# Kernel optimization log

Hardware: AMD Instinct MI355X
Metric: run time of the kernel (lower is better)

The kernel has to match this reference:

```python
import jax, jax.numpy as jnp
import numpy as np

B, S, D_IN, D_OUT = 4, 2048, 4096, 4096
QMAX = 16  # 2**bits

def setup_inputs() -> dict:
    key = jax.random.key(0)
    k1, k2, k3, k4, k5 = jax.random.split(key, 5)
    x = jax.random.normal(k1, (B, S, D_IN), dtype=jnp.float32)
    weight_q = jax.random.randint(k2, (D_OUT, D_IN), 0, QMAX, dtype=jnp.int32)
    scale = jax.random.uniform(k3, (), dtype=jnp.float32) * 0.01 + 1e-4
    zero_point = jax.random.uniform(k4, (), dtype=jnp.float32) * QMAX
    bias = jax.random.normal(k5, (D_OUT,), dtype=jnp.float32)
    return {"x": x, "weight_q": weight_q, "scale": scale,
            "zero_point": zero_point, "bias": bias}

def reference(x, weight_q, scale, zero_point, bias):
    # Dequantize: w = (q - zero_point) * scale, then y = x @ w.T + b
    w = (weight_q.astype(jnp.float32) - zero_point) * scale  # [out, in]
    return jnp.einsum('bsi,oi->bso', x, w) + bias
```

## Files before the change

kernel.cpp:

```cpp
#include <hip/hip_runtime.h>
#include <cstdint>

#define M_DIM 8192
#define N_DIM 4096
#define K_DIM 4096
#define NT    32

typedef int i32x4 __attribute__((ext_vector_type(4)));

__device__ __forceinline__ void gload_lds16(const void* g, void* l) {
  __builtin_amdgcn_global_load_lds(
      (const __attribute__((address_space(1))) unsigned int*)(uintptr_t)g,
      (__attribute__((address_space(3))) unsigned int*)(uintptr_t)l,
      16, 0, 0);
}

__global__ __launch_bounds__(256) void prep_kernel(
    const float* __restrict__ x, const int* __restrict__ q,
    signed char* __restrict__ xq, signed char* __restrict__ wq8,
    float* __restrict__ sx, float* __restrict__ si) {
  const int tid  = threadIdx.x;
  const int lane = tid & 63;
  const int wv   = tid >> 6;
  if (blockIdx.x < 2048) {
    const int row = blockIdx.x * 4 + wv;
    const float* xr = x + (size_t)row * K_DIM;
    signed char* xo = xq + (size_t)row * K_DIM;
    float4 v[16];
    float amax = 0.f;
#pragma unroll
    for (int j = 0; j < 16; ++j) {
      v[j] = *(const float4*)(xr + j * 256 + lane * 4);
      amax = fmaxf(amax, fmaxf(fmaxf(fabsf(v[j].x), fabsf(v[j].y)),
                               fmaxf(fabsf(v[j].z), fabsf(v[j].w))));
    }
#pragma unroll
    for (int off = 32; off > 0; off >>= 1)
      amax = fmaxf(amax, __shfl_xor(amax, off, 64));
    const float inv = amax > 0.f ? 127.f / amax : 0.f;
    int isum = 0;
#pragma unroll
    for (int j = 0; j < 16; ++j) {
      int ix = __float2int_rn(v[j].x * inv);
      int iy = __float2int_rn(v[j].y * inv);
      int iz = __float2int_rn(v[j].z * inv);
      int iw = __float2int_rn(v[j].w * inv);
      isum += ix + iy + iz + iw;
      char4 o; o.x = (char)ix; o.y = (char)iy; o.z = (char)iz; o.w = (char)iw;
      *(char4*)(xo + j * 256 + lane * 4) = o;
    }
#pragma unroll
    for (int off = 32; off > 0; off >>= 1)
      isum += __shfl_xor(isum, off, 64);
    if (lane == 0) {
      sx[row] = amax * (1.f / 127.f);
      si[row] = (float)isum;
    }
  } else {
    const int bid = blockIdx.x - 2048;
    const size_t total  = (size_t)N_DIM * K_DIM;
    const size_t stride = (size_t)1024 * 4096;
    for (size_t base = (size_t)bid * 4096; base < total; base += stride) {
#pragma unroll
      for (int u = 0; u < 4; ++u) {
        const size_t idx = base + (size_t)u * 1024 + tid * 4;
        int4 w = *(const int4*)(q + idx);
        char4 o; o.x = (char)w.x; o.y = (char)w.y; o.z = (char)w.z; o.w = (char)w.w;
        *(char4*)(wq8 + idx) = o;
      }
    }
  }
}

__global__ __launch_bounds__(512, 2) void qlinear_gemm_kernel(
    const signed char* __restrict__ A,
    const signed char* __restrict__ Bm,
    const float* __restrict__ sx,
    const float* __restrict__ si,
    const float* __restrict__ scale_p, const float* __restrict__ zp_p,
    const float* __restrict__ bias,
    float* __restrict__ out) {
  __shared__ signed char sA[2][2][16384];
  __shared__ signed char sB[2][2][16384];

  const int tid  = threadIdx.x;
  const int lane = tid & 63;
  const int w    = tid >> 6;
  const int wr   = w >> 2;
  const int wc   = w & 3;
  const int lr   = lane & 15;
  const int quad = lane >> 4;

  const int bid = blockIdx.x;
  const int swz = (bid & 7) * 64 + (bid >> 3);
  const int bm  = (swz >> 4) * 256;
  const int bn  = (swz & 15) * 256;

  const int srow = lane >> 3;
  const int cg   = (lane & 7) ^ srow;
  const signed char* aG = A  + (size_t)(bm + w * 8 + srow) * K_DIM + cg * 16;
  const signed char* bG = Bm + (size_t)(bn + w * 8 + srow) * K_DIM + cg * 16;
  const int dwoff = w * 1024;

#define STG_A(dst, h, c, t) \
  gload_lds16(aG + (size_t)((h) * 128 + (c) * 64) * K_DIM + (size_t)(t) * 128, \
              (dst) + (h) * 16384 + (c) * 8192 + dwoff)
#define STG_B(dst, h, c, t) \
  gload_lds16(bG + (size_t)((h) * 128 + (c) * 64) * K_DIM + (size_t)(t) * 128, \
              (dst) + (h) * 16384 + (c) * 8192 + dwoff)

  int off[2];
#pragma unroll
  for (int ks = 0; ks < 2; ++ks)
    off[ks] = lr * 128 + (((ks * 4 + quad) ^ (lr & 7)) * 16);

  i32x4 acc[8][4] = {};

  {
    signed char* dA = &sA[0][0][0];
    signed char* dB = &sB[0][0][0];
    STG_B(dB, 0, 0, 0); STG_B(dB, 0, 1, 0);
    STG_B(dB, 1, 0, 0); STG_B(dB, 1, 1, 0);
    STG_A(dA, 0, 0, 0); STG_A(dA, 1, 0, 0);
    STG_A(dA, 0, 1, 0); STG_A(dA, 1, 1, 0);
  }
  asm volatile("s_waitcnt vmcnt(0)" ::: "memory");
  __builtin_amdgcn_s_barrier();

  for (int t = 0; t < NT; ++t) {
    const int buf = t & 1;
    const signed char* pA = &sA[buf][wr][0];
    const signed char* pB = &sB[buf][wc >> 1][0] + (wc & 1) * 8192;
    signed char* nA = &sA[buf ^ 1][0][0];
    signed char* nB = &sB[buf ^ 1][0][0];
    const bool st = (t + 1) < NT;
    const int tn = t + 1;

    if (st) {
      STG_B(nB, 0, 0, tn); STG_B(nB, 0, 1, tn);
      STG_B(nB, 1, 0, tn); STG_B(nB, 1, 1, tn);
      STG_A(nA, 0, 0, tn); STG_A(nA, 1, 0, tn);
      STG_A(nA, 0, 1, tn); STG_A(nA, 1, 1, tn);
    }
    __builtin_amdgcn_sched_barrier(0);

    i32x4 bfr[4][2], afr[4][2];
#pragma unroll
    for (int n = 0; n < 4; ++n)
#pragma unroll
      for (int ks = 0; ks < 2; ++ks)
        bfr[n][ks] = *(const i32x4*)(pB + n * 2048 + off[ks]);
#pragma unroll
    for (int m = 0; m < 4; ++m)
#pragma unroll
      for (int ks = 0; ks < 2; ++ks)
        afr[m][ks] = *(const i32x4*)(pA + m * 2048 + off[ks]);

#pragma unroll
    for (int m = 0; m < 4; ++m)
#pragma unroll
      for (int n = 0; n < 4; ++n)
#pragma unroll
        for (int ks = 0; ks < 2; ++ks)
          acc[m][n] = __builtin_amdgcn_mfma_i32_16x16x64_i8(
              afr[m][ks], bfr[n][ks], acc[m][n], 0, 0, 0);

    i32x4 afr2[4][2];
#pragma unroll
    for (int m = 0; m < 4; ++m)
#pragma unroll
      for (int ks = 0; ks < 2; ++ks)
        afr2[m][ks] = *(const i32x4*)(pA + 8192 + m * 2048 + off[ks]);

#pragma unroll
    for (int m = 0; m < 4; ++m)
#pragma unroll
      for (int n = 0; n < 4; ++n)
#pragma unroll
        for (int ks = 0; ks < 2; ++ks)
          acc[4 + m][n] = __builtin_amdgcn_mfma_i32_16x16x64_i8(
              afr2[m][ks], bfr[n][ks], acc[4 + m][n], 0, 0, 0);

    if (st) {
      asm volatile("s_waitcnt vmcnt(0)" ::: "memory");
      __builtin_amdgcn_s_barrier();
    }
  }
#undef STG_A
#undef STG_B

  const float scale = *scale_p;
  const float zp    = *zp_p;
#pragma unroll
  for (int i = 0; i < 8; ++i) {
    const int gm0 = bm + wr * 128 + i * 16 + quad * 4;
    float am[4], cm[4];
#pragma unroll
    for (int r = 0; r < 4; ++r) {
      am[r] = scale * sx[gm0 + r];
      cm[r] = -am[r] * zp * si[gm0 + r];
    }
#pragma unroll
    for (int j = 0; j < 4; ++j) {
      const int gn = bn + wc * 64 + j * 16 + lr;
      const float bb = bias[gn];
#pragma unroll
      for (int r = 0; r < 4; ++r)
        out[(size_t)(gm0 + r) * N_DIM + gn] =
            am[r] * (float)acc[i][j][r] + cm[r] + bb;
    }
  }
}

extern "C" void kernel_launch(void* const* d_in, const int* in_sizes, int n_in,
                              void* d_out, int out_size, void* d_ws, size_t ws_size,
                              hipStream_t stream) {
  const float* x     = (const float*)d_in[0];
  const int*   wq    = (const int*)d_in[1];
  const float* scale = (const float*)d_in[2];
  const float* zp    = (const float*)d_in[3];
  const float* bias  = (const float*)d_in[4];
  float* out = (float*)d_out;

  signed char* xq  = (signed char*)d_ws;
  signed char* wq8 = xq + (size_t)M_DIM * K_DIM;
  float* sx = (float*)(wq8 + (size_t)N_DIM * K_DIM);
  float* si = sx + M_DIM;

  prep_kernel<<<3072, 256, 0, stream>>>(x, wq, xq, wq8, sx, si);
  qlinear_gemm_kernel<<<512, 512, 0, stream>>>(xq, wq8, sx, si, scale, zp, bias, out);
}
```

Baseline: 391.7 us.

## Interleave staged global loads with MFMA sub-phases using partial waitcnt and setprio

Splits each K-tile iteration into eight MFMA sub-blocks. Each sub-block is preceded by a small batch of LDS fragment reads and one global-to-LDS load for the next tile, guarded by a barrier and a partial vmcnt wait instead of one full wait at the end. It also raises wave priority around MFMA groups and drops the XCD-aware block swizzle in favor of a plain 2D grid. The goal is to overlap memory traffic with matrix math and cut register pressure from holding all fragments at once. In exchange it adds many more barriers per iteration, and the partial waits make correctness depend on the ordering of the outstanding loads.

```diff
diff --git a/kernel.cpp b/kernel.cpp
--- a/kernel.cpp
+++ b/kernel.cpp
@@ -91,10 +91,8 @@
   const int lr   = lane & 15;
   const int quad = lane >> 4;
 
-  const int bid = blockIdx.x;
-  const int swz = (bid & 7) * 64 + (bid >> 3);
-  const int bm  = (swz >> 4) * 256;
-  const int bn  = (swz & 15) * 256;
+  const int bm = blockIdx.y * 256;
+  const int bn = blockIdx.x * 256;
 
   const int srow = lane >> 3;
   const int cg   = (lane & 7) ^ srow;
@@ -115,6 +113,7 @@
     off[ks] = lr * 128 + (((ks * 4 + quad) ^ (lr & 7)) * 16);
 
   i32x4 acc[8][4] = {};
+  i32x4 afrA[4], afrB[4], bfr0[2], bfr1[2];
 
   {
     signed char* dA = &sA[0][0][0];
@@ -124,7 +123,7 @@
     STG_A(dA, 0, 0, 0); STG_A(dA, 1, 0, 0);
     STG_A(dA, 0, 1, 0); STG_A(dA, 1, 1, 0);
   }
-  asm volatile("s_waitcnt vmcnt(0)" ::: "memory");
+  asm volatile("s_waitcnt vmcnt(2)" ::: "memory");
   __builtin_amdgcn_s_barrier();
 
   for (int t = 0; t < NT; ++t) {
@@ -136,55 +135,67 @@
     const bool st = (t + 1) < NT;
     const int tn = t + 1;
 
-    if (st) {
-      STG_B(nB, 0, 0, tn); STG_B(nB, 0, 1, tn);
-      STG_B(nB, 1, 0, tn); STG_B(nB, 1, 1, tn);
-      STG_A(nA, 0, 0, tn); STG_A(nA, 1, 0, tn);
-      STG_A(nA, 0, 1, tn); STG_A(nA, 1, 1, tn);
-    }
-    __builtin_amdgcn_sched_barrier(0);
-
-    i32x4 bfr[4][2], afr[4][2];
-#pragma unroll
-    for (int n = 0; n < 4; ++n)
-#pragma unroll
-      for (int ks = 0; ks < 2; ++ks)
-        bfr[n][ks] = *(const i32x4*)(pB + n * 2048 + off[ks]);
-#pragma unroll
-    for (int m = 0; m < 4; ++m)
-#pragma unroll
-      for (int ks = 0; ks < 2; ++ks)
-        afr[m][ks] = *(const i32x4*)(pA + m * 2048 + off[ks]);
-
-#pragma unroll
-    for (int m = 0; m < 4; ++m)
-#pragma unroll
-      for (int n = 0; n < 4; ++n)
-#pragma unroll
-        for (int ks = 0; ks < 2; ++ks)
-          acc[m][n] = __builtin_amdgcn_mfma_i32_16x16x64_i8(
-              afr[m][ks], bfr[n][ks], acc[m][n], 0, 0, 0);
-
-    i32x4 afr2[4][2];
-#pragma unroll
-    for (int m = 0; m < 4; ++m)
-#pragma unroll
-      for (int ks = 0; ks < 2; ++ks)
-        afr2[m][ks] = *(const i32x4*)(pA + 8192 + m * 2048 + off[ks]);
-
-#pragma unroll
-    for (int m = 0; m < 4; ++m)
-#pragma unroll
-      for (int n = 0; n < 4; ++n)
-#pragma unroll
-        for (int ks = 0; ks < 2; ++ks)
-          acc[4 + m][n] = __builtin_amdgcn_mfma_i32_16x16x64_i8(
-              afr2[m][ks], bfr[n][ks], acc[4 + m][n], 0, 0, 0);
-
-    if (st) {
-      asm volatile("s_waitcnt vmcnt(0)" ::: "memory");
-      __builtin_amdgcn_s_barrier();
-    }
+#define MFMA8(AF, BF, MB, NB)                                              \
+  __builtin_amdgcn_s_setprio(1);                                           \
+  _Pragma("unroll")                                                        \
+  for (int m = 0; m < 4; ++m)                                              \
+    _Pragma("unroll")                                                      \
+    for (int n = 0; n < 2; ++n)                                            \
+      acc[(MB) + m][(NB) + n] = __builtin_amdgcn_mfma_i32_16x16x64_i8(     \
+          AF[m], BF[n], acc[(MB) + m][(NB) + n], 0, 0, 0);                 \
+  __builtin_amdgcn_s_setprio(0);
+
+#pragma unroll
+    for (int m = 0; m < 4; ++m) afrA[m] = *(const i32x4*)(pA + m * 2048 + off[0]);
+#pragma unroll
+    for (int n = 0; n < 2; ++n) bfr0[n] = *(const i32x4*)(pB + n * 2048 + off[0]);
+    if (st) STG_B(nB, 0, 0, tn);
+    __builtin_amdgcn_s_barrier();
+    MFMA8(afrA, bfr0, 0, 0)
+
+#pragma unroll
+    for (int n = 0; n < 2; ++n) bfr1[n] = *(const i32x4*)(pB + 4096 + n * 2048 + off[0]);
+    if (st) { STG_B(nB, 0, 1, tn);
+              asm volatile("s_waitcnt vmcnt(2)" ::: "memory"); }
+    else      asm volatile("s_waitcnt vmcnt(0)" ::: "memory");
+    __builtin_amdgcn_s_barrier();
+    MFMA8(afrA, bfr1, 0, 2)
+
+#pragma unroll
+    for (int m = 0; m < 4; ++m) afrB[m] = *(const i32x4*)(pA + 8192 + m * 2048 + off[0]);
+    if (st) STG_B(nB, 1, 0, tn);
+    __builtin_amdgcn_s_barrier();
+    MFMA8(afrB, bfr0, 4, 0)
+
+    if (st) STG_B(nB, 1, 1, tn);
+    __builtin_amdgcn_s_barrier();
+    MFMA8(afrB, bfr1, 4, 2)
+
+#pragma unroll
+    for (int m = 0; m < 4; ++m) afrA[m] = *(const i32x4*)(pA + m * 2048 + off[1]);
+#pragma unroll
+    for (int n = 0; n < 2; ++n) bfr0[n] = *(const i32x4*)(pB + n * 2048 + off[1]);
+    if (st) STG_A(nA, 0, 0, tn);
+    __builtin_amdgcn_s_barrier();
+    MFMA8(afrA, bfr0, 0, 0)
+
+#pragma unroll
+    for (int n = 0; n < 2; ++n) bfr1[n] = *(const i32x4*)(pB + 4096 + n * 2048 + off[1]);
+    if (st) STG_A(nA, 1, 0, tn);
+    __builtin_amdgcn_s_barrier();
+    MFMA8(afrA, bfr1, 0, 2)
+
+#pragma unroll
+    for (int m = 0; m < 4; ++m) afrB[m] = *(const i32x4*)(pA + 8192 + m * 2048 + off[1]);
+    if (st) STG_A(nA, 0, 1, tn);
+    __builtin_amdgcn_s_barrier();
+    MFMA8(afrB, bfr0, 4, 0)
+
+    if (st) { STG_A(nA, 1, 1, tn);
+              asm volatile("s_waitcnt vmcnt(2)" ::: "memory"); }
+    __builtin_amdgcn_s_barrier();
+    MFMA8(afrB, bfr1, 4, 2)
+#undef MFMA8
   }
 #undef STG_A
 #undef STG_B
@@ -228,5 +239,6 @@
   float* si = sx + M_DIM;
 
   prep_kernel<<<3072, 256, 0, stream>>>(x, wq, xq, wq8, sx, si);
-  qlinear_gemm_kernel<<<512, 512, 0, stream>>>(xq, wq8, sx, si, scale, zp, bias, out);
-}
+  dim3 grid(N_DIM / 256, M_DIM / 256);
+  qlinear_gemm_kernel<<<grid, 512, 0, stream>>>(xq, wq8, sx, si, scale, zp, bias, out);
+}
```

After: 382.6 us. 2.3% less time.
